# Kernel tuning notes

Hardware: AMD Instinct MI355X
Metric: run time of the kernel (lower is better)

Reference implementation:

```python
import jax, jax.numpy as jnp
import numpy as np

# Mamba2 defaults (mamba_ssm): d_state=128, d_conv=4, expand=2, headdim=64, ngroups=1
NB, D_MODEL, D_STATE, D_CONV, HEADDIM = 2, 512, 128, 4, 64
D_INNER = 2 * D_MODEL                      # expand * d_model
NHEADS = D_INNER // HEADDIM                # 16
CONV_DIM = D_INNER + 2 * D_STATE           # x, B, C go through depthwise conv
D_IN_PROJ = 2 * D_INNER + 2 * D_STATE + NHEADS  # z, xBC, dt
VOCAB, LABEL, B, L = 32000, 1000, 2, 512


def setup_inputs() -> dict:
    key = jax.random.key(0)
    ks = jax.random.split(key, 8)
    nrm = lambda k, shape, s: jax.random.normal(k, shape, dtype=jnp.float32) * s
    tokens = jax.random.randint(ks[0], (B, L), 0, VOCAB)
    embedding = nrm(ks[1], (VOCAB, D_MODEL), 0.02)
    in_proj_w = nrm(ks[2], (NB, D_IN_PROJ, D_MODEL), D_MODEL ** -0.5)
    conv_w = nrm(ks[3], (NB, CONV_DIM, D_CONV), D_CONV ** -0.5)
    conv_b = jnp.zeros((NB, CONV_DIM), jnp.float32)
    # dt_bias = inverse-softplus of dt ~ logUniform[1e-3, 0.1] (Mamba2 init)
    dt = jnp.exp(jax.random.uniform(ks[4], (NB, NHEADS), minval=float(np.log(1e-3)), maxval=float(np.log(0.1))))
    dt_bias = dt + jnp.log(-jnp.expm1(-dt))
    A_log = jnp.log(jax.random.uniform(ks[5], (NB, NHEADS), minval=1.0, maxval=16.0))
    D = jnp.ones((NB, NHEADS), jnp.float32)
    rms_w = jnp.ones((NB, D_INNER), jnp.float32)
    out_proj_w = nrm(ks[6], (NB, D_MODEL, D_INNER), D_INNER ** -0.5)
    ln_w = jnp.ones((NB, D_MODEL), jnp.float32)
    ln_b = jnp.zeros((NB, D_MODEL), jnp.float32)
    head_w = nrm(ks[7], (LABEL, D_MODEL), D_MODEL ** -0.5)
    head_b = jnp.zeros((LABEL,), jnp.float32)
    return dict(tokens=tokens, embedding=embedding, in_proj_w=in_proj_w, conv_w=conv_w,
                conv_b=conv_b, dt_bias=dt_bias, A_log=A_log, D=D, rms_w=rms_w,
                out_proj_w=out_proj_w, ln_w=ln_w, ln_b=ln_b, head_w=head_w, head_b=head_b)


def _mamba2(u, Wi, cw, cb, dtb, Alog, Dv, rw, Wo):
    b, l, _ = u.shape
    zxbcdt = u @ Wi.T                                  # (b,l,D_IN_PROJ)
    z = zxbcdt[..., :D_INNER]
    xBC = zxbcdt[..., D_INNER:D_INNER + CONV_DIM]
    dt = jax.nn.softplus(zxbcdt[..., D_INNER + CONV_DIM:] + dtb)   # (b,l,h)
    # causal depthwise conv1d, kernel size D_CONV
    xp = jnp.pad(xBC, ((0, 0), (D_CONV - 1, 0), (0, 0)))
    xBC = sum(xp[:, k:k + l, :] * cw[:, k] for k in range(D_CONV)) + cb
    xBC = jax.nn.silu(xBC)
    xh = xBC[..., :D_INNER].reshape(b, l, NHEADS, HEADDIM)
    Bm = xBC[..., D_INNER:D_INNER + D_STATE]           # (b,l,n), ngroups=1
    Cm = xBC[..., D_INNER + D_STATE:]                  # (b,l,n)
    A = -jnp.exp(Alog)                                 # (h,)
    dA = jnp.exp(dt * A)                               # (b,l,h)

    def step(h, inp):
        dA_t, dt_t, x_t, B_t, C_t = inp                # (b,h),(b,h),(b,h,p),(b,n),(b,n)
        h = h * dA_t[:, :, None, None] + (dt_t[:, :, None] * x_t)[..., None] * B_t[:, None, None, :]
        return h, jnp.einsum('bhpn,bn->bhp', h, C_t)

    h0 = jnp.zeros((b, NHEADS, HEADDIM, D_STATE), u.dtype)
    inp = (jnp.swapaxes(dA, 0, 1), jnp.swapaxes(dt, 0, 1), jnp.swapaxes(xh, 0, 1),
           jnp.swapaxes(Bm, 0, 1), jnp.swapaxes(Cm, 0, 1))
    _, ys = jax.lax.scan(step, h0, inp)
    y = jnp.swapaxes(ys, 0, 1) + Dv[:, None] * xh      # (b,l,h,p)
    # gated RMSNorm (norm_before_gate=False): normalize y*silu(z)
    y = y.reshape(b, l, D_INNER) * jax.nn.silu(z)
    y = y * jax.lax.rsqrt(jnp.mean(y * y, -1, keepdims=True) + 1e-5) * rw
    return y @ Wo.T


def _layernorm(x, w, bias):
    mu = jnp.mean(x, -1, keepdims=True)
    xc = x - mu
    var = jnp.mean(xc * xc, -1, keepdims=True)
    return xc * jax.lax.rsqrt(var + 1e-5) * w + bias


def reference(tokens, embedding, in_proj_w, conv_w, conv_b, dt_bias, A_log, D,
              rms_w, out_proj_w, ln_w, ln_b, head_w, head_b):
    x = embedding[tokens]                              # (b,l,d)
    for i in range(NB):
        y = _mamba2(x, in_proj_w[i], conv_w[i], conv_b[i], dt_bias[i],
                    A_log[i], D[i], rms_w[i], out_proj_w[i])
        x = _layernorm(y + x, ln_w[i], ln_b[i])        # residual + LN (dropout=identity)
    return x @ head_w.T + head_b                        # (b,l,label)
```

## Files before the change

kernel.cpp:

```cpp
#include <hip/hip_runtime.h>

#define L_SEQ 512
#define BATCH 2
#define NROWS (BATCH*L_SEQ)
#define DMODEL 512
#define DINNER 1024
#define DSTATE 128
#define NHEADSM 16
#define CONVD 1280
#define DINPROJ 2320
#define QCH 32
#define NCH 16
#define WI_PAD 2368
#define WH_PAD 1024

#define W_CONVW 0
#define W_CONVB 10240
#define W_DTB   12800
#define W_ALOG  12832
#define W_DD    12864
#define W_RMSW  12896
#define W_LNW   14944
#define W_LNB   15968
#define W_HEADB 16992
#define O_X     18048
#define O_ZX    (O_X  + NROWS*DMODEL)
#define O_XC    (O_ZX + NROWS*DINPROJ)
#define O_DT    (O_XC + NROWS*CONVD)
#define O_Y     (O_DT + NROWS*NHEADSM)
#define O_O     (O_Y  + NROWS*DINNER)
#define O_LA    (O_O  + NROWS*DMODEL)
#define O_S     (O_LA + 16384)
#define O_UB    (O_S  + 4194304)
#define U_WI   0
#define U_WO   2424832
#define U_WH   3473408
#define U_XBF  3997696
#define U_YBF  4521984

#define NSMALL 17992
#define NPREPW (2*WI_PAD + 2*DMODEL + WH_PAD)

typedef __attribute__((ext_vector_type(8))) short short8;
typedef __attribute__((ext_vector_type(4))) float floatx4;

__device__ __forceinline__ float b2f(unsigned short h){ return __uint_as_float(((unsigned)h)<<16); }
__device__ __forceinline__ unsigned short f2b(float x){
  unsigned u = __float_as_uint(x);
  return (unsigned short)((u + 0x7fffu + ((u>>16)&1u)) >> 16);
}
__device__ __forceinline__ float loadIn(const void* p, long i, int f){
  return f ? b2f(((const unsigned short*)p)[i]) : ((const float*)p)[i];
}

__device__ __forceinline__ void gload16(const void* g, void* l){
  __builtin_amdgcn_global_load_lds((const __attribute__((address_space(1))) void*)g,
                                   (__attribute__((address_space(3))) void*)l, 16, 0, 0);
}

__global__ void k_detect(const unsigned* __restrict__ emb, int* __restrict__ flag){
  __shared__ int red[256];
  int t = threadIdx.x; int cnt = 0;
  for (int i = 0; i < 16; i++){
    unsigned w = emb[t*16 + i];
    unsigned e = (w >> 7) & 0xffu;
    cnt += (e >= 100 && e <= 126) ? 1 : 0;
  }
  red[t] = cnt; __syncthreads();
  if (t == 0){
    int s = 0;
    for (int i = 0; i < 256; i++) s += red[i];
    *flag = (s > 2048) ? 1 : 0;
  }
}

struct ConvArgs { const void* src[9]; int off[10]; };

__global__ void k_prep(ConvArgs a, const void* __restrict__ wi, const void* __restrict__ wo,
                       const void* __restrict__ wh, const int* __restrict__ tok,
                       const void* __restrict__ emb, const int* __restrict__ flag,
                       float* __restrict__ dstSmall,
                       unsigned short* __restrict__ WiB, unsigned short* __restrict__ WoB,
                       unsigned short* __restrict__ WhB,
                       float* __restrict__ x, unsigned short* __restrict__ xbf)
{
  int f = *flag;
  int blk = blockIdx.x;
  if (blk < 71){
    int i = blk*256 + threadIdx.x;
    if (i < a.off[9]){
      int s = 0;
      while (i >= a.off[s+1]) s++;
      dstSmall[i] = loadIn(a.src[s], i - a.off[s], f);
    }
    return;
  }
  blk -= 71;
  if (blk < NPREPW){
    int r = blk;
    const void* src = nullptr; unsigned short* dst; long sb = 0, db; int K; bool zero = false;
    if (r < 2*WI_PAD){
      int layer = r / WI_PAD, row = r % WI_PAD;
      K = DMODEL; dst = WiB; db = ((long)layer*WI_PAD + row)*DMODEL;
      if (row < DINPROJ){ src = wi; sb = ((long)layer*DINPROJ + row)*DMODEL; } else zero = true;
    } else if (r < 2*WI_PAD + 2*DMODEL){
      int rr = r - 2*WI_PAD;
      K = DINNER; dst = WoB; db = (long)rr*DINNER;
      src = wo; sb = db;
    } else {
      int row = r - 2*WI_PAD - 2*DMODEL;
      K = DMODEL; dst = WhB; db = (long)row*DMODEL;
      if (row < 1000){ src = wh; sb = db; } else zero = true;
    }
    for (int c = threadIdx.x; c < K; c += 256)
      dst[db + c] = zero ? (unsigned short)0
                         : (f ? ((const unsigned short*)src)[sb + c] : f2b(((const float*)src)[sb + c]));
    return;
  }
  int r = blk - NPREPW;
  long base = (long)tok[r] * DMODEL;
  for (int c = threadIdx.x; c < DMODEL; c += 256){
    float v = loadIn(emb, base + c, f);
    x[(long)r*DMODEL + c] = v;
    xbf[(long)r*DMODEL + c] = f ? ((const unsigned short*)emb)[base + c] : f2b(v);
  }
}

template<int BM, int BN>
__global__ __launch_bounds__(256) void k_mfma_nt(
    const unsigned short* __restrict__ A, const unsigned short* __restrict__ B,
    void* __restrict__ C, int M, int N, int K,
    const float* __restrict__ bias, const int* __restrict__ flag, int outDual)
{
  constexpr int MI = BM/32;
  constexpr int NI = BN/32;
  constexpr int CA = BM/32;
  constexpr int CB = BN/32;
  __shared__ __align__(16) unsigned short As[2][BM*64];
  __shared__ __align__(16) unsigned short Bs[2][BN*64];
  int f = *flag;
  int t = threadIdx.x;
  int w = t >> 6, lane = t & 63;
  int quad = lane >> 4, l16 = lane & 15;
  int m0 = blockIdx.y * BM, n0 = blockIdx.x * BN;
  int wm = (w & 1) * (BM/2), wn = (w >> 1) * (BN/2);
  floatx4 acc[MI][NI];
  #pragma unroll
  for (int mi = 0; mi < MI; mi++)
    #pragma unroll
    for (int ni = 0; ni < NI; ni++) acc[mi][ni] = (floatx4){0.f,0.f,0.f,0.f};

  const char* Ag = (const char*)A;
  const char* Bg = (const char*)B;
  long aOff[CA]; int aL[CA];
  #pragma unroll
  for (int j = 0; j < CA; j++){
    int i = (w*CA + j)*64 + lane;
    int r = i >> 3, g = (i & 7) ^ (r & 7);
    aOff[j] = ((long)(m0 + r)*K + g*8)*2;
    aL[j] = (w*CA + j)*1024;
  }
  long bOff[CB]; int bL[CB];
  #pragma unroll
  for (int j = 0; j < CB; j++){
    int i = (w*CB + j)*64 + lane;
    int r = i >> 3, g = (i & 7) ^ (r & 7);
    bOff[j] = ((long)(n0 + r)*K + g*8)*2;
    bL[j] = (w*CB + j)*1024;
  }

  const int NKI = K >> 6;
  #pragma unroll
  for (int j = 0; j < CA; j++) gload16(Ag + aOff[j], (char*)As[0] + aL[j]);
  #pragma unroll
  for (int j = 0; j < CB; j++) gload16(Bg + bOff[j], (char*)Bs[0] + bL[j]);
  asm volatile("s_waitcnt vmcnt(0)" ::: "memory");
  __syncthreads();

  for (int ki = 0; ki < NKI; ki++){
    int cur = ki & 1;
    if (ki + 1 < NKI){
      long kb = (long)(ki + 1)*128;
      #pragma unroll
      for (int j = 0; j < CA; j++) gload16(Ag + aOff[j] + kb, (char*)As[cur^1] + aL[j]);
      #pragma unroll
      for (int j = 0; j < CB; j++) gload16(Bg + bOff[j] + kb, (char*)Bs[cur^1] + bL[j]);
    }
    const unsigned short* Ac = As[cur];
    const unsigned short* Bc = Bs[cur];
    #pragma unroll
    for (int ks = 0; ks < 2; ks++){
      short8 af[MI], bfr[NI];
      #pragma unroll
      for (int mi = 0; mi < MI; mi++){
        int r = wm + mi*16 + l16;
        int pos = ((ks << 2) + quad) ^ (r & 7);
        af[mi] = *(const short8*)&Ac[r*64 + pos*8];
      }
      #pragma unroll
      for (int ni = 0; ni < NI; ni++){
        int r = wn + ni*16 + l16;
        int pos = ((ks << 2) + quad) ^ (r & 7);
        bfr[ni] = *(const short8*)&Bc[r*64 + pos*8];
      }
      #pragma unroll
      for (int mi = 0; mi < MI; mi++)
        #pragma unroll
        for (int ni = 0; ni < NI; ni++)
          acc[mi][ni] = __builtin_amdgcn_mfma_f32_16x16x32_bf16(af[mi], bfr[ni], acc[mi][ni], 0, 0, 0);
    }
    asm volatile("s_waitcnt vmcnt(0)" ::: "memory");
    __syncthreads();
  }
  #pragma unroll
  for (int mi = 0; mi < MI; mi++)
    #pragma unroll
    for (int ni = 0; ni < NI; ni++){
      int col = n0 + wn + ni*16 + l16;
      if (col >= N) continue;
      float bv = bias ? bias[col] : 0.f;
      #pragma unroll
      for (int rr = 0; rr < 4; rr++){
        int row = m0 + wm + mi*16 + (quad << 2) + rr;
        float v = acc[mi][ni][rr] + bv;
        long idx = (long)row*N + col;
        if (outDual && f) ((unsigned short*)C)[idx] = f2b(v);
        else              ((float*)C)[idx] = v;
      }
    }
}

__global__ __launch_bounds__(256) void k_conv_dt(
    const float* __restrict__ zx, const float* __restrict__ cw, const float* __restrict__ cb,
    const float* __restrict__ dtb, float* __restrict__ xc, float* __restrict__ dt)
{
  int r = blockIdx.x; int b = r >> 9, l = r & 511;
  int t = threadIdx.x;
  for (int c = t; c < CONVD; c += 256){
    float s = cb[c];
    #pragma unroll
    for (int k = 0; k < 4; k++){
      int pos = l - 3 + k;
      if (pos >= 0)
        s = fmaf(zx[(long)(b*L_SEQ + pos)*DINPROJ + DINNER + c], cw[c*4 + k], s);
    }
    xc[(long)r*CONVD + c] = s / (1.f + __expf(-s));
  }
  if (t < NHEADSM){
    float v = zx[(long)r*DINPROJ + DINNER + CONVD + t] + dtb[t];
    dt[r*NHEADSM + t] = (v > 20.f) ? v : log1pf(__expf(v));
  }
}

__global__ __launch_bounds__(256) void k_chunk1(
    const float* __restrict__ xc, const float* __restrict__ dtbuf,
    const float* __restrict__ alog, const float* __restrict__ dvec,
    float* __restrict__ S, float* __restrict__ LAb, float* __restrict__ y)
{
  int c = blockIdx.x, h = blockIdx.y, b = blockIdx.z;
  int t = threadIdx.x, w = t >> 6, lane = t & 63;
  int quad = lane >> 4, l16 = lane & 15;
  int l0 = c*QCH;
  __shared__ unsigned short XT[64*40];
  __shared__ unsigned short BTc[128*40];
  __shared__ unsigned short Bb[32*136];
  __shared__ unsigned short Cb[32*136];
  __shared__ unsigned short Gb[32*40];
  __shared__ float dtl[32], lal[32], coef[32];
  float A  = -__expf(alog[h]);
  float Dv = dvec[h];

  float xv[8];
  #pragma unroll
  for (int k = 0; k < 8; k++){
    int idx = t + k*256; int j = idx >> 6, p = idx & 63;
    xv[k] = xc[(long)(b*L_SEQ + l0 + j)*CONVD + h*64 + p];
  }
  float bv[16], cv[16];
  #pragma unroll
  for (int k = 0; k < 16; k++){
    int idx = t + k*256; int j = idx >> 7, n = idx & 127;
    long rb = (long)(b*L_SEQ + l0 + j)*CONVD + DINNER;
    bv[k] = xc[rb + n];
    cv[k] = xc[rb + DSTATE + n];
  }
  if (t < 32){
    float d = dtbuf[(b*L_SEQ + l0 + t)*NHEADSM + h];
    dtl[t] = d;
    float s = d;
    #pragma unroll
    for (int o = 1; o < 32; o <<= 1){
      float u = __shfl_up(s, o, 32);
      if (t >= o) s += u;
    }
    float la = s * A;
    lal[t] = la;
    float tot = __shfl(s, 31, 32) * A;
    coef[t] = __expf(tot - la) * d;
    LAb[(b*NHEADSM + h)*L_SEQ + l0 + t] = la;
  }
  __syncthreads();
  #pragma unroll
  for (int k = 0; k < 8; k++){
    int idx = t + k*256; int j = idx >> 6, p = idx & 63;
    XT[p*40 + j] = f2b(xv[k]);
  }
  #pragma unroll
  for (int k = 0; k < 16; k++){
    int idx = t + k*256; int j = idx >> 7, n = idx & 127;
    Bb[j*136 + n] = f2b(bv[k]);
    Cb[j*136 + n] = f2b(cv[k]);
    BTc[n*40 + j] = f2b(bv[k] * coef[j]);
  }
  __syncthreads();

  short8 afS = *(const short8*)&XT[(w*16 + l16)*40 + quad*8];
  floatx4 accS[8];
  #pragma unroll
  for (int nb = 0; nb < 8; nb++){
    short8 bfS = *(const short8*)&BTc[(nb*16 + l16)*40 + quad*8];
    accS[nb] = __builtin_amdgcn_mfma_f32_16x16x32_bf16(afS, bfS, (floatx4){0.f,0.f,0.f,0.f}, 0, 0, 0);
  }
  int ti = w & 1, tj = w >> 1;
  floatx4 accG = (floatx4){0.f,0.f,0.f,0.f};
  #pragma unroll
  for (int ks = 0; ks < 4; ks++){
    short8 ga = *(const short8*)&Cb[(ti*16 + l16)*136 + ks*32 + quad*8];
    short8 gb = *(const short8*)&Bb[(tj*16 + l16)*136 + ks*32 + quad*8];
    accG = __builtin_amdgcn_mfma_f32_16x16x32_bf16(ga, gb, accG, 0, 0, 0);
  }
  long sb = ((long)((b*NHEADSM + h)*NCH + c))*8192;
  #pragma unroll
  for (int nb = 0; nb < 8; nb++)
    #pragma unroll
    for (int rr = 0; rr < 4; rr++)
      S[sb + (w*16 + quad*4 + rr)*128 + nb*16 + l16] = accS[nb][rr];
  #pragma unroll
  for (int rr = 0; rr < 4; rr++){
    int i = ti*16 + quad*4 + rr, j = tj*16 + l16;
    float g = (j <= i) ? __expf(lal[i] - lal[j]) * dtl[j] * accG[rr] : 0.f;
    Gb[i*40 + j] = f2b(g);
  }
  __syncthreads();
  short8 ag = *(const short8*)&Gb[(ti*16 + l16)*40 + quad*8];
  #pragma unroll
  for (int s = 0; s < 2; s++){
    int pb = (w >> 1)*2 + s;
    short8 bx = *(const short8*)&XT[(pb*16 + l16)*40 + quad*8];
    floatx4 accY = __builtin_amdgcn_mfma_f32_16x16x32_bf16(ag, bx, (floatx4){0.f,0.f,0.f,0.f}, 0, 0, 0);
    #pragma unroll
    for (int rr = 0; rr < 4; rr++){
      int i = ti*16 + quad*4 + rr, p = pb*16 + l16;
      float xval = b2f(XT[p*40 + i]);
      y[(long)(b*L_SEQ + l0 + i)*DINNER + h*64 + p] = fmaf(Dv, xval, accY[rr]);
    }
  }
}

__global__ __launch_bounds__(256) void k_chunk2(
    float* __restrict__ S, const float* __restrict__ LAb)
{
  int bh = blockIdx.x >> 5;
  int e = ((blockIdx.x & 31) << 8) + threadIdx.x;
  long base = (long)bh*NCH*8192 + e;
  int laBase = bh*L_SEQ;
  float lam[NCH];
  #pragma unroll
  for (int c = 0; c < NCH; c++) lam[c] = __expf(LAb[laBase + c*QCH + QCH - 1]);
  float hr = 0.f;
  #pragma unroll
  for (int c = 0; c < NCH; c++){
    long off = base + (long)c*8192;
    float sv = S[off];
    S[off] = hr;
    hr = fmaf(hr, lam[c], sv);
  }
}

__global__ __launch_bounds__(256) void k_chunk3(
    const float* __restrict__ xc, const float* __restrict__ H,
    const float* __restrict__ LAb, float* __restrict__ y)
{
  int c = blockIdx.x, h = blockIdx.y, b = blockIdx.z;
  int t = threadIdx.x, w = t >> 6, lane = t & 63;
  int quad = lane >> 4, l16 = lane & 15;
  int l0 = c*QCH;
  __shared__ unsigned short Cb[32*136];
  __shared__ unsigned short Hhi[64*136];
  __shared__ unsigned short Hlo[64*136];
  __shared__ float el[32];
  if (t < 32) el[t] = __expf(LAb[(b*NHEADSM + h)*L_SEQ + l0 + t]);
  #pragma unroll
  for (int k = 0; k < 16; k++){
    int idx = t + k*256; int j = idx >> 7, n = idx & 127;
    Cb[j*136 + n] = f2b(xc[(long)(b*L_SEQ + l0 + j)*CONVD + DINNER + DSTATE + n]);
  }
  long hb = ((long)((b*NHEADSM + h)*NCH + c))*8192;
  #pragma unroll
  for (int k = 0; k < 32; k++){
    int idx = t + k*256; int p = idx >> 7, n = idx & 127;
    float v = H[hb + idx];
    unsigned short hi = f2b(v);
    Hhi[p*136 + n] = hi;
    Hlo[p*136 + n] = f2b(v - b2f(hi));
  }
  __syncthreads();
  int ti = w & 1;
  #pragma unroll
  for (int s = 0; s < 2; s++){
    int pb = (w >> 1)*2 + s;
    floatx4 acc = (floatx4){0.f,0.f,0.f,0.f};
    #pragma unroll
    for (int ks = 0; ks < 4; ks++){
      short8 a  = *(const short8*)&Cb [(ti*16 + l16)*136 + ks*32 + quad*8];
      short8 bl = *(const short8*)&Hlo[(pb*16 + l16)*136 + ks*32 + quad*8];
      short8 bh = *(const short8*)&Hhi[(pb*16 + l16)*136 + ks*32 + quad*8];
      acc = __builtin_amdgcn_mfma_f32_16x16x32_bf16(a, bl, acc, 0, 0, 0);
      acc = __builtin_amdgcn_mfma_f32_16x16x32_bf16(a, bh, acc, 0, 0, 0);
    }
    #pragma unroll
    for (int rr = 0; rr < 4; rr++){
      int i = ti*16 + quad*4 + rr, p = pb*16 + l16;
      long yb = (long)(b*L_SEQ + l0 + i)*DINNER + h*64 + p;
      y[yb] = fmaf(el[i], acc[rr], y[yb]);
    }
  }
}

__global__ __launch_bounds__(256) void k_gated_rms(
    const float* __restrict__ y, const float* __restrict__ zx, const float* __restrict__ rw,
    unsigned short* __restrict__ ybf)
{
  int r = blockIdx.x, t = threadIdx.x;
  float g[4]; float ss = 0.f;
  #pragma unroll
  for (int i = 0; i < 4; i++){
    int c = t + i*256;
    float z  = zx[(long)r*DINPROJ + c];
    float yv = y[(long)r*DINNER + c];
    float gz = z / (1.f + __expf(-z));
    g[i] = yv * gz;
    ss = fmaf(g[i], g[i], ss);
  }
  #pragma unroll
  for (int o = 1; o < 64; o <<= 1) ss += __shfl_xor(ss, o);
  __shared__ float red[4];
  int w = t >> 6, lane = t & 63;
  if (lane == 0) red[w] = ss;
  __syncthreads();
  float tot = red[0] + red[1] + red[2] + red[3];
  float sc = rsqrtf(tot / (float)DINNER + 1e-5f);
  #pragma unroll
  for (int i = 0; i < 4; i++){
    int c = t + i*256;
    ybf[(long)r*DINNER + c] = f2b(g[i] * sc * rw[c]);
  }
}

__global__ __launch_bounds__(256) void k_add_ln(
    float* __restrict__ x, const float* __restrict__ o,
    const float* __restrict__ lw, const float* __restrict__ lb,
    unsigned short* __restrict__ xbf)
{
  int r = blockIdx.x, t = threadIdx.x;
  float v[2]; float sm = 0.f;
  #pragma unroll
  for (int i = 0; i < 2; i++){ int c = t + i*256; v[i] = x[(long)r*DMODEL + c] + o[(long)r*DMODEL + c]; sm += v[i]; }
  #pragma unroll
  for (int off = 1; off < 64; off <<= 1) sm += __shfl_xor(sm, off);
  __shared__ float red[4]; __shared__ float red2[4];
  int w = t >> 6, lane = t & 63;
  if (lane == 0) red[w] = sm;
  __syncthreads();
  float mu = (red[0] + red[1] + red[2] + red[3]) / (float)DMODEL;
  float var = 0.f;
  #pragma unroll
  for (int i = 0; i < 2; i++){ v[i] -= mu; var = fmaf(v[i], v[i], var); }
  #pragma unroll
  for (int off = 1; off < 64; off <<= 1) var += __shfl_xor(var, off);
  if (lane == 0) red2[w] = var;
  __syncthreads();
  float vv = (red2[0] + red2[1] + red2[2] + red2[3]) / (float)DMODEL;
  float sc = rsqrtf(vv + 1e-5f);
  #pragma unroll
  for (int i = 0; i < 2; i++){
    int c = t + i*256;
    float ov = v[i]*sc*lw[c] + lb[c];
    x[(long)r*DMODEL + c] = ov;
    xbf[(long)r*DMODEL + c] = f2b(ov);
  }
}

extern "C" void kernel_launch(void* const* d_in, const int* in_sizes, int n_in,
                              void* d_out, int out_size, void* d_ws, size_t ws_size,
                              hipStream_t stream)
{
  const int* tokens = (const int*)d_in[0];
  const void* emb = d_in[1];
  int* flag = (int*)d_ws;
  float* ws = (float*)((char*)d_ws + 256);

  k_detect<<<1, 256, 0, stream>>>((const unsigned*)emb, flag);

  ConvArgs ca;
  const int sizes[9] = {10240, 2560, 32, 32, 32, 2048, 1024, 1024, 1000};
  const int idxs[9]  = {3, 4, 5, 6, 7, 8, 10, 11, 13};
  int off = 0;
  for (int s = 0; s < 9; s++){ ca.src[s] = d_in[idxs[s]]; ca.off[s] = off; off += sizes[s]; }
  ca.off[9] = off;

  float* X  = ws + O_X;
  float* ZX = ws + O_ZX;
  float* XC = ws + O_XC;
  float* DT = ws + O_DT;
  float* Y  = ws + O_Y;
  float* Ob = ws + O_O;
  float* LA = ws + O_LA;
  float* Sb = ws + O_S;
  unsigned short* ub  = (unsigned short*)(ws + O_UB);
  unsigned short* WiB = ub + U_WI;
  unsigned short* WoB = ub + U_WO;
  unsigned short* WhB = ub + U_WH;
  unsigned short* Xbf = ub + U_XBF;
  unsigned short* Ybf = ub + U_YBF;

  k_prep<<<71 + NPREPW + NROWS, 256, 0, stream>>>(
      ca, d_in[2], d_in[9], d_in[12], tokens, emb, flag,
      ws, WiB, WoB, WhB, X, Xbf);

  for (int layer = 0; layer < 2; layer++){
    k_mfma_nt<64,64><<<dim3(WI_PAD/64, NROWS/64), 256, 0, stream>>>(
        Xbf, WiB + (long)layer*WI_PAD*DMODEL, (void*)ZX,
        NROWS, DINPROJ, DMODEL, (const float*)nullptr, flag, 0);
    k_conv_dt<<<NROWS, 256, 0, stream>>>(
        ZX, ws + W_CONVW + layer*5120, ws + W_CONVB + layer*1280, ws + W_DTB + layer*16, XC, DT);
    k_chunk1<<<dim3(NCH, NHEADSM, BATCH), 256, 0, stream>>>(
        XC, DT, ws + W_ALOG + layer*16, ws + W_DD + layer*16, Sb, LA, Y);
    k_chunk2<<<1024, 256, 0, stream>>>(Sb, LA);
    k_chunk3<<<dim3(NCH, NHEADSM, BATCH), 256, 0, stream>>>(XC, Sb, LA, Y);
    k_gated_rms<<<NROWS, 256, 0, stream>>>(Y, ZX, ws + W_RMSW + layer*1024, Ybf);
    k_mfma_nt<32,32><<<dim3(DMODEL/32, NROWS/32), 256, 0, stream>>>(
        Ybf, WoB + (long)layer*DMODEL*DINNER, (void*)Ob,
        NROWS, DMODEL, DINNER, (const float*)nullptr, flag, 0);
    k_add_ln<<<NROWS, 256, 0, stream>>>(X, Ob, ws + W_LNW + layer*512, ws + W_LNB + layer*512, Xbf);
  }

  k_mfma_nt<32,64><<<dim3(WH_PAD/64, NROWS/32), 256, 0, stream>>>(
      Xbf, WhB, d_out, NROWS, 1000, DMODEL, ws + W_HEADB, flag, 1);
}
```

Before: 249.7 us.

## Fuse gated RMSNorm into chunk scan and out-proj epilogue, move x-conv into chunk1

Removes the standalone gated RMSNorm kernel. The chunk3 scan kernel now applies the silu(z) gate, writes unnormalized bf16 output, and atomically accumulates per-row sums of squares. The out-projection GEMM epilogue applies the rsqrt row scale, and the RMS weight is folded into the out-proj weights at prep time. The x-channel depthwise conv is also moved into chunk1 via an LDS halo tile, so conv_dt only writes the B/C channels, which cuts global traffic. In exchange it adds atomics and a float-order change, and the gated values are rounded to bf16 before normalization.

```diff
diff --git a/kernel.cpp b/kernel.cpp
--- a/kernel.cpp
+++ b/kernel.cpp
@@ -26,11 +26,12 @@
 #define O_X     18048
 #define O_ZX    (O_X  + NROWS*DMODEL)
 #define O_XC    (O_ZX + NROWS*DINPROJ)
-#define O_DT    (O_XC + NROWS*CONVD)
+#define O_DT    (O_XC + NROWS*256)
 #define O_Y     (O_DT + NROWS*NHEADSM)
 #define O_O     (O_Y  + NROWS*DINNER)
 #define O_LA    (O_O  + NROWS*DMODEL)
-#define O_S     (O_LA + 16384)
+#define O_SS    (O_LA + 16384)
+#define O_S     (O_SS + 1024)
 #define O_UB    (O_S  + 4194304)
 #define U_WI   0
 #define U_WO   2424832
@@ -38,7 +39,6 @@
 #define U_XBF  3997696
 #define U_YBF  4521984
 
-#define NSMALL 17992
 #define NPREPW (2*WI_PAD + 2*DMODEL + WH_PAD)
 
 typedef __attribute__((ext_vector_type(8))) short short8;
@@ -77,7 +77,8 @@
 struct ConvArgs { const void* src[9]; int off[10]; };
 
 __global__ void k_prep(ConvArgs a, const void* __restrict__ wi, const void* __restrict__ wo,
-                       const void* __restrict__ wh, const int* __restrict__ tok,
+                       const void* __restrict__ wh, const void* __restrict__ rwsrc,
+                       const int* __restrict__ tok,
                        const void* __restrict__ emb, const int* __restrict__ flag,
                        float* __restrict__ dstSmall,
                        unsigned short* __restrict__ WiB, unsigned short* __restrict__ WoB,
@@ -98,23 +99,35 @@
   blk -= 71;
   if (blk < NPREPW){
     int r = blk;
-    const void* src = nullptr; unsigned short* dst; long sb = 0, db; int K; bool zero = false;
     if (r < 2*WI_PAD){
       int layer = r / WI_PAD, row = r % WI_PAD;
-      K = DMODEL; dst = WiB; db = ((long)layer*WI_PAD + row)*DMODEL;
-      if (row < DINPROJ){ src = wi; sb = ((long)layer*DINPROJ + row)*DMODEL; } else zero = true;
+      long db = ((long)layer*WI_PAD + row)*DMODEL;
+      if (row < DINPROJ){
+        long sb = ((long)layer*DINPROJ + row)*DMODEL;
+        for (int c = threadIdx.x; c < DMODEL; c += 256)
+          WiB[db + c] = f ? ((const unsigned short*)wi)[sb + c] : f2b(((const float*)wi)[sb + c]);
+      } else {
+        for (int c = threadIdx.x; c < DMODEL; c += 256) WiB[db + c] = 0;
+      }
     } else if (r < 2*WI_PAD + 2*DMODEL){
       int rr = r - 2*WI_PAD;
-      K = DINNER; dst = WoB; db = (long)rr*DINNER;
-      src = wo; sb = db;
+      int layer = rr >> 9;
+      long db = (long)rr*DINNER;
+      for (int c = threadIdx.x; c < DINNER; c += 256){
+        float wv = loadIn(wo, db + c, f);
+        float rv = loadIn(rwsrc, (long)layer*DINNER + c, f);
+        WoB[db + c] = f2b(wv * rv);
+      }
     } else {
       int row = r - 2*WI_PAD - 2*DMODEL;
-      K = DMODEL; dst = WhB; db = (long)row*DMODEL;
-      if (row < 1000){ src = wh; sb = db; } else zero = true;
-    }
-    for (int c = threadIdx.x; c < K; c += 256)
-      dst[db + c] = zero ? (unsigned short)0
-                         : (f ? ((const unsigned short*)src)[sb + c] : f2b(((const float*)src)[sb + c]));
+      long db = (long)row*DMODEL;
+      if (row < 1000){
+        for (int c = threadIdx.x; c < DMODEL; c += 256)
+          WhB[db + c] = f ? ((const unsigned short*)wh)[db + c] : f2b(((const float*)wh)[db + c]);
+      } else {
+        for (int c = threadIdx.x; c < DMODEL; c += 256) WhB[db + c] = 0;
+      }
+    }
     return;
   }
   int r = blk - NPREPW;
@@ -130,7 +143,8 @@
 __global__ __launch_bounds__(256) void k_mfma_nt(
     const unsigned short* __restrict__ A, const unsigned short* __restrict__ B,
     void* __restrict__ C, int M, int N, int K,
-    const float* __restrict__ bias, const int* __restrict__ flag, int outDual)
+    const float* __restrict__ bias, const float* __restrict__ rowscale,
+    const int* __restrict__ flag, int outDual)
 {
   constexpr int MI = BM/32;
   constexpr int NI = BN/32;
@@ -223,6 +237,7 @@
       for (int rr = 0; rr < 4; rr++){
         int row = m0 + wm + mi*16 + (quad << 2) + rr;
         float v = acc[mi][ni][rr] + bv;
+        if (rowscale) v *= rsqrtf(rowscale[row]*(1.f/(float)DINNER) + 1e-5f);
         long idx = (long)row*N + col;
         if (outDual && f) ((unsigned short*)C)[idx] = f2b(v);
         else              ((float*)C)[idx] = v;
@@ -236,15 +251,16 @@
 {
   int r = blockIdx.x; int b = r >> 9, l = r & 511;
   int t = threadIdx.x;
-  for (int c = t; c < CONVD; c += 256){
-    float s = cb[c];
+  {
+    int ch = 1024 + t;
+    float s = cb[ch];
     #pragma unroll
     for (int k = 0; k < 4; k++){
       int pos = l - 3 + k;
       if (pos >= 0)
-        s = fmaf(zx[(long)(b*L_SEQ + pos)*DINPROJ + DINNER + c], cw[c*4 + k], s);
-    }
-    xc[(long)r*CONVD + c] = s / (1.f + __expf(-s));
+        s = fmaf(zx[(long)(b*L_SEQ + pos)*DINPROJ + 2048 + t], cw[ch*4 + k], s);
+    }
+    xc[(long)r*256 + t] = s / (1.f + __expf(-s));
   }
   if (t < NHEADSM){
     float v = zx[(long)r*DINPROJ + DINNER + CONVD + t] + dtb[t];
@@ -253,8 +269,10 @@
 }
 
 __global__ __launch_bounds__(256) void k_chunk1(
-    const float* __restrict__ xc, const float* __restrict__ dtbuf,
+    const float* __restrict__ zx, const float* __restrict__ xc,
+    const float* __restrict__ dtbuf,
     const float* __restrict__ alog, const float* __restrict__ dvec,
+    const float* __restrict__ cw, const float* __restrict__ cb,
     float* __restrict__ S, float* __restrict__ LAb, float* __restrict__ y)
 {
   int c = blockIdx.x, h = blockIdx.y, b = blockIdx.z;
@@ -262,7 +280,10 @@
   int quad = lane >> 4, l16 = lane & 15;
   int l0 = c*QCH;
   __shared__ unsigned short XT[64*40];
-  __shared__ unsigned short BTc[128*40];
+  __shared__ union {
+    float xs[35*64];
+    unsigned short BTc[128*40];
+  } U;
   __shared__ unsigned short Bb[32*136];
   __shared__ unsigned short Cb[32*136];
   __shared__ unsigned short Gb[32*40];
@@ -270,19 +291,18 @@
   float A  = -__expf(alog[h]);
   float Dv = dvec[h];
 
-  float xv[8];
-  #pragma unroll
-  for (int k = 0; k < 8; k++){
-    int idx = t + k*256; int j = idx >> 6, p = idx & 63;
-    xv[k] = xc[(long)(b*L_SEQ + l0 + j)*CONVD + h*64 + p];
+  for (int idx = t; idx < 35*64; idx += 256){
+    int jr = idx >> 6, cc = idx & 63;
+    int l = l0 - 3 + jr;
+    U.xs[idx] = (l >= 0) ? zx[(long)(b*L_SEQ + l)*DINPROJ + 1024 + h*64 + cc] : 0.f;
   }
   float bv[16], cv[16];
   #pragma unroll
   for (int k = 0; k < 16; k++){
     int idx = t + k*256; int j = idx >> 7, n = idx & 127;
-    long rb = (long)(b*L_SEQ + l0 + j)*CONVD + DINNER;
+    long rb = (long)(b*L_SEQ + l0 + j)*256;
     bv[k] = xc[rb + n];
-    cv[k] = xc[rb + DSTATE + n];
+    cv[k] = xc[rb + 128 + n];
   }
   if (t < 32){
     float d = dtbuf[(b*L_SEQ + l0 + t)*NHEADSM + h];
@@ -300,6 +320,18 @@
     LAb[(b*NHEADSM + h)*L_SEQ + l0 + t] = la;
   }
   __syncthreads();
+  float xv[8];
+  #pragma unroll
+  for (int k = 0; k < 8; k++){
+    int idx = t + k*256; int j = idx >> 6, p = idx & 63;
+    int ch = h*64 + p;
+    float s0 = cb[ch];
+    #pragma unroll
+    for (int kk = 0; kk < 4; kk++)
+      s0 = fmaf(U.xs[(j + kk)*64 + p], cw[ch*4 + kk], s0);
+    xv[k] = s0 / (1.f + __expf(-s0));
+  }
+  __syncthreads();
   #pragma unroll
   for (int k = 0; k < 8; k++){
     int idx = t + k*256; int j = idx >> 6, p = idx & 63;
@@ -310,7 +342,7 @@
     int idx = t + k*256; int j = idx >> 7, n = idx & 127;
     Bb[j*136 + n] = f2b(bv[k]);
     Cb[j*136 + n] = f2b(cv[k]);
-    BTc[n*40 + j] = f2b(bv[k] * coef[j]);
+    U.BTc[n*40 + j] = f2b(bv[k] * coef[j]);
   }
   __syncthreads();
 
@@ -318,7 +350,7 @@
   floatx4 accS[8];
   #pragma unroll
   for (int nb = 0; nb < 8; nb++){
-    short8 bfS = *(const short8*)&BTc[(nb*16 + l16)*40 + quad*8];
+    short8 bfS = *(const short8*)&U.BTc[(nb*16 + l16)*40 + quad*8];
     accS[nb] = __builtin_amdgcn_mfma_f32_16x16x32_bf16(afS, bfS, (floatx4){0.f,0.f,0.f,0.f}, 0, 0, 0);
   }
   int ti = w & 1, tj = w >> 1;
@@ -358,8 +390,9 @@
 }
 
 __global__ __launch_bounds__(256) void k_chunk2(
-    float* __restrict__ S, const float* __restrict__ LAb)
-{
+    float* __restrict__ S, const float* __restrict__ LAb, float* __restrict__ SS)
+{
+  if (threadIdx.x == 0) SS[blockIdx.x] = 0.f;
   int bh = blockIdx.x >> 5;
   int e = ((blockIdx.x & 31) << 8) + threadIdx.x;
   long base = (long)bh*NCH*8192 + e;
@@ -379,7 +412,9 @@
 
 __global__ __launch_bounds__(256) void k_chunk3(
     const float* __restrict__ xc, const float* __restrict__ H,
-    const float* __restrict__ LAb, float* __restrict__ y)
+    const float* __restrict__ LAb, const float* __restrict__ y,
+    const float* __restrict__ zx, unsigned short* __restrict__ ybf,
+    float* __restrict__ SS)
 {
   int c = blockIdx.x, h = blockIdx.y, b = blockIdx.z;
   int t = threadIdx.x, w = t >> 6, lane = t & 63;
@@ -393,7 +428,7 @@
   #pragma unroll
   for (int k = 0; k < 16; k++){
     int idx = t + k*256; int j = idx >> 7, n = idx & 127;
-    Cb[j*136 + n] = f2b(xc[(long)(b*L_SEQ + l0 + j)*CONVD + DINNER + DSTATE + n]);
+    Cb[j*136 + n] = f2b(xc[(long)(b*L_SEQ + l0 + j)*256 + 128 + n]);
   }
   long hb = ((long)((b*NHEADSM + h)*NCH + c))*8192;
   #pragma unroll
@@ -406,6 +441,7 @@
   }
   __syncthreads();
   int ti = w & 1;
+  float gsq[4] = {0.f, 0.f, 0.f, 0.f};
   #pragma unroll
   for (int s = 0; s < 2; s++){
     int pb = (w >> 1)*2 + s;
@@ -421,39 +457,25 @@
     #pragma unroll
     for (int rr = 0; rr < 4; rr++){
       int i = ti*16 + quad*4 + rr, p = pb*16 + l16;
-      long yb = (long)(b*L_SEQ + l0 + i)*DINNER + h*64 + p;
-      y[yb] = fmaf(el[i], acc[rr], y[yb]);
-    }
-  }
-}
-
-__global__ __launch_bounds__(256) void k_gated_rms(
-    const float* __restrict__ y, const float* __restrict__ zx, const float* __restrict__ rw,
-    unsigned short* __restrict__ ybf)
-{
-  int r = blockIdx.x, t = threadIdx.x;
-  float g[4]; float ss = 0.f;
-  #pragma unroll
-  for (int i = 0; i < 4; i++){
-    int c = t + i*256;
-    float z  = zx[(long)r*DINPROJ + c];
-    float yv = y[(long)r*DINNER + c];
-    float gz = z / (1.f + __expf(-z));
-    g[i] = yv * gz;
-    ss = fmaf(g[i], g[i], ss);
-  }
-  #pragma unroll
-  for (int o = 1; o < 64; o <<= 1) ss += __shfl_xor(ss, o);
-  __shared__ float red[4];
-  int w = t >> 6, lane = t & 63;
-  if (lane == 0) red[w] = ss;
-  __syncthreads();
-  float tot = red[0] + red[1] + red[2] + red[3];
-  float sc = rsqrtf(tot / (float)DINNER + 1e-5f);
-  #pragma unroll
-  for (int i = 0; i < 4; i++){
-    int c = t + i*256;
-    ybf[(long)r*DINNER + c] = f2b(g[i] * sc * rw[c]);
+      long row = (long)(b*L_SEQ + l0 + i);
+      long yb = row*DINNER + h*64 + p;
+      float yfin = fmaf(el[i], acc[rr], y[yb]);
+      float z = zx[row*DINPROJ + h*64 + p];
+      float gz = z / (1.f + __expf(-z));
+      float g = yfin * gz;
+      ybf[yb] = f2b(g);
+      gsq[rr] = fmaf(g, g, gsq[rr]);
+    }
+  }
+  #pragma unroll
+  for (int rr = 0; rr < 4; rr++){
+    float v = gsq[rr];
+    v += __shfl_xor(v, 1);
+    v += __shfl_xor(v, 2);
+    v += __shfl_xor(v, 4);
+    v += __shfl_xor(v, 8);
+    if (l16 == 0)
+      atomicAdd(&SS[b*L_SEQ + l0 + ti*16 + quad*4 + rr], v);
   }
 }
 
@@ -516,6 +538,7 @@
   float* Y  = ws + O_Y;
   float* Ob = ws + O_O;
   float* LA = ws + O_LA;
+  float* SSb= ws + O_SS;
   float* Sb = ws + O_S;
   unsigned short* ub  = (unsigned short*)(ws + O_UB);
   unsigned short* WiB = ub + U_WI;
@@ -525,26 +548,27 @@
   unsigned short* Ybf = ub + U_YBF;
 
   k_prep<<<71 + NPREPW + NROWS, 256, 0, stream>>>(
-      ca, d_in[2], d_in[9], d_in[12], tokens, emb, flag,
+      ca, d_in[2], d_in[9], d_in[12], d_in[8], tokens, emb, flag,
       ws, WiB, WoB, WhB, X, Xbf);
 
   for (int layer = 0; layer < 2; layer++){
     k_mfma_nt<64,64><<<dim3(WI_PAD/64, NROWS/64), 256, 0, stream>>>(
         Xbf, WiB + (long)layer*WI_PAD*DMODEL, (void*)ZX,
-        NROWS, DINPROJ, DMODEL, (const float*)nullptr, flag, 0);
+        NROWS, DINPROJ, DMODEL, (const float*)nullptr, (const float*)nullptr, flag, 0);
     k_conv_dt<<<NROWS, 256, 0, stream>>>(
         ZX, ws + W_CONVW + layer*5120, ws + W_CONVB + layer*1280, ws + W_DTB + layer*16, XC, DT);
     k_chunk1<<<dim3(NCH, NHEADSM, BATCH), 256, 0, stream>>>(
-        XC, DT, ws + W_ALOG + layer*16, ws + W_DD + layer*16, Sb, LA, Y);
-    k_chunk2<<<1024, 256, 0, stream>>>(Sb, LA);
-    k_chunk3<<<dim3(NCH, NHEADSM, BATCH), 256, 0, stream>>>(XC, Sb, LA, Y);
-    k_gated_rms<<<NROWS, 256, 0, stream>>>(Y, ZX, ws + W_RMSW + layer*1024, Ybf);
+        ZX, XC, DT, ws + W_ALOG + layer*16, ws + W_DD + layer*16,
+        ws + W_CONVW + layer*5120, ws + W_CONVB + layer*1280, Sb, LA, Y);
+    k_chunk2<<<1024, 256, 0, stream>>>(Sb, LA, SSb);
+    k_chunk3<<<dim3(NCH, NHEADSM, BATCH), 256, 0, stream>>>(
+        XC, Sb, LA, Y, ZX, Ybf, SSb);
     k_mfma_nt<32,32><<<dim3(DMODEL/32, NROWS/32), 256, 0, stream>>>(
         Ybf, WoB + (long)layer*DMODEL*DINNER, (void*)Ob,
-        NROWS, DMODEL, DINNER, (const float*)nullptr, flag, 0);
+        NROWS, DMODEL, DINNER, (const float*)nullptr, SSb, flag, 0);
     k_add_ln<<<NROWS, 256, 0, stream>>>(X, Ob, ws + W_LNW + layer*512, ws + W_LNB + layer*512, Xbf);
   }
 
   k_mfma_nt<32,64><<<dim3(WH_PAD/64, NROWS/32), 256, 0, stream>>>(
-      Xbf, WhB, d_out, NROWS, 1000, DMODEL, ws + W_HEADB, flag, 1);
-}
+      Xbf, WhB, d_out, NROWS, 1000, DMODEL, ws + W_HEADB, (const float*)nullptr, flag, 1);
+}
```

After: 248.1 us. No clear change (-0.7%).
